# Optimization experiments

Hardware: AMD Instinct MI355X
Metric: run time of the kernel (lower is better)

## Reference

```python
import jax, jax.numpy as jnp
import numpy as np

H = 16
D_MODEL = 1024
D_K = D_MODEL // H


def setup_inputs() -> dict:
    key = jax.random.key(0)
    ks = jax.random.split(key, 8)
    B, S = 4, 2048
    query = jax.random.normal(ks[0], (B, S, D_MODEL), dtype=jnp.float32)
    key_t = jax.random.normal(ks[1], (B, S, D_MODEL), dtype=jnp.float32)
    value = jax.random.normal(ks[2], (B, S, D_MODEL), dtype=jnp.float32)
    mask = jax.random.randint(ks[3], (B, S, S), 0, 2, dtype=jnp.int32)
    sc = 1.0 / np.sqrt(D_MODEL)
    Wq = jax.random.normal(ks[4], (D_MODEL, D_MODEL), dtype=jnp.float32) * sc
    Wk = jax.random.normal(ks[5], (D_MODEL, D_MODEL), dtype=jnp.float32) * sc
    Wv = jax.random.normal(ks[6], (D_MODEL, D_MODEL), dtype=jnp.float32) * sc
    Wo = jax.random.normal(ks[7], (D_MODEL, D_MODEL), dtype=jnp.float32) * sc
    return {"query": query, "key": key_t, "value": value, "mask": mask,
            "Wq": Wq, "Wk": Wk, "Wv": Wv, "Wo": Wo}


def reference(query, key, value, mask, Wq, Wk, Wv, Wo):
    B, S, _ = query.shape
    # nn.Linear(bias=False): y = x @ W^T; then split heads -> [B,H,S,d_k]
    def proj(x, W):
        return (x @ W.T).reshape(B, S, H, D_K).transpose(0, 2, 1, 3)

    q = proj(query, Wq)
    k = proj(key, Wk)
    v = proj(value, Wv)

    m = (mask[:, None, :, :] != 0)  # [B,1,S,S] broadcast over heads
    scores = jnp.einsum('bhqd,bhkd->bhqk', q, k) / jnp.sqrt(jnp.float32(D_K))
    scores = jnp.where(m, scores, jnp.float32(-1e9))
    p_attn = jax.nn.softmax(scores, axis=-1)
    p_attn = jnp.where(m, p_attn, 0.0)
    # dropout is identity in eval mode
    x = jnp.einsum('bhqk,bhkd->bhqd', p_attn, v)
    x = x.transpose(0, 2, 1, 3).reshape(B, S, D_MODEL)
    return x @ Wo.T
```

## Files before the change

### kernel.cpp

```cpp
#include <hip/hip_runtime.h>


typedef __attribute__((ext_vector_type(8))) short frag8;
typedef __attribute__((ext_vector_type(4))) float f32x4;
typedef unsigned long long ull;

#define MFMA16(a,b,c) __builtin_amdgcn_mfma_f32_16x16x32_bf16((a),(b),(c),0,0,0)

__device__ __forceinline__ short f2bf(float f) {
  union { float f; unsigned u; } x; x.f = f;
  unsigned r = (x.u + 0x7fffu + ((x.u >> 16) & 1u)) >> 16;
  return (short)r;
}

__device__ __forceinline__ unsigned pkbf(float lo, float hi) {
  union { float f; unsigned u; } a, b;
  a.f = lo; b.f = hi;
  return __builtin_amdgcn_perm(b.u + 0x8000u, a.u + 0x8000u, 0x07060302u);
}

__device__ __forceinline__ void gl16(const void* g, void* l) {
  __builtin_amdgcn_global_load_lds(
      (const __attribute__((address_space(1))) unsigned*)g,
      (__attribute__((address_space(3))) unsigned*)l, 16, 0, 0);
}

__global__ __launch_bounds__(256) void cast_qkv(
    const float* __restrict__ q, const float* __restrict__ k,
    const float* __restrict__ v, short* __restrict__ qo,
    short* __restrict__ ko, short* __restrict__ vo) {
  int z = blockIdx.x >> 13;
  int i = (blockIdx.x & 8191) * 256 + threadIdx.x;
  const float* s = z == 0 ? q : z == 1 ? k : v;
  short* d = z == 0 ? qo : z == 1 ? ko : vo;
  float4 f = ((const float4*)s)[i];
  short4 o;
  o.x = f2bf(f.x); o.y = f2bf(f.y); o.z = f2bf(f.z); o.w = f2bf(f.w);
  ((short4*)d)[i] = o;
}

__global__ __launch_bounds__(256) void cast_w(
    const float* __restrict__ wq, const float* __restrict__ wk,
    const float* __restrict__ wv, const float* __restrict__ wo,
    short* __restrict__ oq, short* __restrict__ ok,
    short* __restrict__ ov, short* __restrict__ oo) {
  int z = blockIdx.x >> 10;
  int i = (blockIdx.x & 1023) * 256 + threadIdx.x;
  const float* s = z == 0 ? wq : z == 1 ? wk : z == 2 ? wv : wo;
  short* d = z == 0 ? oq : z == 1 ? ok : z == 2 ? ov : oo;
  float sc = (z == 0) ? 0.18033688011f : 1.0f;
  float4 f = ((const float4*)s)[i];
  short4 o;
  o.x = f2bf(f.x * sc); o.y = f2bf(f.y * sc);
  o.z = f2bf(f.z * sc); o.w = f2bf(f.w * sc);
  ((short4*)d)[i] = o;
}

__global__ __launch_bounds__(256) void mask_expand(
    const int* __restrict__ mask, uint2* __restrict__ mexp) {
  int bgrp = blockIdx.x >> 2;
  int kq = blockIdx.x & 3;
  int b = bgrp >> 6, g = bgrp & 63;
  int t = threadIdx.x;
  int l = t & 63, nb = t >> 6;
  int lg = l >> 4, lr = l & 15;
#pragma unroll
  for (int qb = 0; qb < 2; ++qb) {
    const int* row = mask + ((size_t)b * 2048 + g * 32 + qb * 16 + lr) * 2048;
#pragma unroll
    for (int i = 0; i < 8; ++i) {
      int kt = kq * 8 + i;
      int4 m = *(const int4*)(row + kt * 64 + nb * 16 + lg * 4);
      uint2 w;
      w.x = (m.x ? 0xFFFFu : 0u) | (m.y ? 0xFFFF0000u : 0u);
      w.y = (m.z ? 0xFFFFu : 0u) | (m.w ? 0xFFFF0000u : 0u);
      mexp[((size_t)bgrp * 32 + kt) * 512 + (qb * 4 + nb) * 64 + l] = w;
    }
  }
}

template <int MODE>
__device__ __forceinline__ void gemm_body(const short* __restrict__ A,
                                          const short* __restrict__ W,
                                          void* __restrict__ outp, int bid) {
  __shared__ short As[2][128 * 32];
  __shared__ short Bs[2][128 * 32];
  const int t = threadIdx.x;
  const int l = t & 63, wv = t >> 6;
  const int lg = l >> 4, lr = l & 15;
  const int wm = (wv >> 1) * 64, wn = (wv & 1) * 64;
  const int m0 = (bid >> 3) * 128;
  const int n0 = (bid & 7) * 128;

  auto stage = [&](int buf, int kt) {
    const int k0 = kt * 32;
#pragma unroll
    for (int c = 0; c < 2; ++c) {
      int idx = c * 256 + t;
      int row = idx >> 2, ch = (idx & 3) * 8;
      gl16(A + (size_t)(m0 + row) * 1024 + k0 + ch, &As[buf][idx * 8]);
      gl16(W + (size_t)(n0 + row) * 1024 + k0 + ch, &Bs[buf][idx * 8]);
    }
  };

  f32x4 acc[4][4] = {};
  stage(0, 0);
  asm volatile("s_waitcnt vmcnt(0)" ::: "memory");
  __syncthreads();
  int buf = 0;
  for (int kt = 0; kt < 32; ++kt) {
    if (kt + 1 < 32) stage(buf ^ 1, kt + 1);
    frag8 af[4], bf[4];
#pragma unroll
    for (int i = 0; i < 4; ++i) {
      af[i] = *(const frag8*)&As[buf][(wm + i * 16 + lr) * 32 + 8 * lg];
      bf[i] = *(const frag8*)&Bs[buf][(wn + i * 16 + lr) * 32 + 8 * lg];
    }
    __builtin_amdgcn_s_setprio(1);
#pragma unroll
    for (int mi = 0; mi < 4; ++mi)
#pragma unroll
      for (int ni = 0; ni < 4; ++ni)
        acc[mi][ni] = MFMA16(af[mi], bf[ni], acc[mi][ni]);
    __builtin_amdgcn_s_setprio(0);
    asm volatile("s_waitcnt vmcnt(0)" ::: "memory");
    __syncthreads();
    buf ^= 1;
  }

#pragma unroll
  for (int mi = 0; mi < 4; ++mi)
#pragma unroll
    for (int ni = 0; ni < 4; ++ni)
#pragma unroll
      for (int r = 0; r < 4; ++r) {
        int m = m0 + wm + mi * 16 + 4 * lg + r;
        int n = n0 + wn + ni * 16 + lr;
        if (MODE == 0) {
          int b = m >> 11, s = m & 2047, h = n >> 6, dk = n & 63;
          ((short*)outp)[(((size_t)b * 16 + h) * 2048 + s) * 64 + dk] =
              f2bf(acc[mi][ni][r]);
        } else {
          ((float*)outp)[(size_t)m * 1024 + n] = acc[mi][ni][r];
        }
      }
}

__global__ __launch_bounds__(256) void gemm_qkv(
    const short* __restrict__ A0, const short* __restrict__ A1,
    const short* __restrict__ A2, const short* __restrict__ W0,
    const short* __restrict__ W1, const short* __restrict__ W2,
    short* __restrict__ O0, short* __restrict__ O1, short* __restrict__ O2) {
  int wg = (blockIdx.x & 7) * 192 + (blockIdx.x >> 3);
  int z = wg >> 9, bid = wg & 511;
  const short* A = z == 0 ? A0 : z == 1 ? A1 : A2;
  const short* W = z == 0 ? W0 : z == 1 ? W1 : W2;
  short* O = z == 0 ? O0 : z == 1 ? O1 : O2;
  gemm_body<0>(A, W, O, bid);
}

__global__ __launch_bounds__(256) void gemm_o(
    const short* __restrict__ A, const short* __restrict__ W,
    float* __restrict__ O) {
  int bid = (blockIdx.x & 7) * 64 + (blockIdx.x >> 3);
  gemm_body<1>(A, W, O, bid);
}

__global__ __launch_bounds__(256) void transpose_v(
    const short* __restrict__ Vp, short* __restrict__ Vt) {
  __shared__ short lds[64 * 72];
  int bh = blockIdx.y, s0 = blockIdx.x * 64;
  int t = threadIdx.x;
  int rr = t >> 3, c0 = (t & 7) * 8;
#pragma unroll
  for (int half = 0; half < 2; ++half) {
    int r = half * 32 + rr;
    frag8 v = *(const frag8*)(Vp + ((size_t)bh * 2048 + s0 + r) * 64 + c0);
#pragma unroll
    for (int j = 0; j < 8; ++j) lds[r * 72 + c0 + j] = v[j];
  }
  __syncthreads();
#pragma unroll
  for (int half = 0; half < 2; ++half) {
    int d = half * 32 + rr;
    frag8 o;
#pragma unroll
    for (int j = 0; j < 8; ++j) o[j] = lds[(c0 + j) * 72 + d];
    *(frag8*)(Vt + ((size_t)bh * 64 + d) * 2048 + s0 + c0) = o;
  }
}

__global__ __launch_bounds__(256, 4) void attn_fwd(
    const short* __restrict__ Qp, const short* __restrict__ Kp,
    const short* __restrict__ Vt, const uint2* __restrict__ mexp,
    short* __restrict__ X) {
  __shared__ short Ks[2][64 * 64];
  __shared__ short Vs[64 * 64];
  __shared__ short Ps[4][32 * 64];

  const int wg = (blockIdx.x & 7) * 128 + (blockIdx.x >> 3);
  const int qt = wg & 15, bh = wg >> 4;
  const int b = bh >> 4, h = bh & 15;
  const int t = threadIdx.x;
  const int l = t & 63, wv = t >> 6;
  const int lg = l >> 4, lr = l & 15;
  const int q0 = qt * 128 + wv * 32;
  const int qrow_base = b << 11;

  frag8 qf[2][2];
  const short* Qb = Qp + ((size_t)bh * 2048 + q0) * 64;
#pragma unroll
  for (int qb = 0; qb < 2; ++qb)
#pragma unroll
    for (int kc = 0; kc < 2; ++kc)
      qf[qb][kc] = *(const frag8*)(Qb + (qb * 16 + lr) * 64 + kc * 32 + 8 * lg);

  f32x4 acc[4][2] = {};
  float mrun[2] = {0.f, 0.f}, lrun[2] = {0.f, 0.f};

  const size_t kbase = (size_t)bh * 2048 * 64;
  const size_t vbase = (size_t)bh * 64 * 2048;
  short* Pw = &Ps[wv][0];
  const int sx = lr & 7;
  const uint2* mrow = mexp + ((size_t)(b * 64 + qt * 4 + wv) * 32) * 512 + l;

  auto stageK = [&](int buf, int kt) {
#pragma unroll
    for (int p = 0; p < 2; ++p) {
      int idx = p * 256 + t;
      int row = idx >> 3, c = idx & 7;
      int cs = (c ^ (row & 7)) * 8;
      gl16(Kp + kbase + (size_t)(kt * 64 + row) * 64 + cs, &Ks[buf][idx * 8]);
    }
  };
  auto stageV = [&](int kt) {
#pragma unroll
    for (int p = 0; p < 2; ++p) {
      int idx = p * 256 + t;
      int row = idx >> 3, c = idx & 7;
      int cs = (c ^ (row & 7)) * 8;
      gl16(Vt + vbase + (size_t)row * 2048 + kt * 64 + cs, &Vs[idx * 8]);
    }
  };

  stageK(0, 0);
  asm volatile("s_waitcnt vmcnt(0)" ::: "memory");
  __syncthreads();
  int buf = 0;

  for (int kt = 0; kt < 32; ++kt) {
    uint2 mk[2][4];
    const uint2* mt = mrow + kt * 512;
#pragma unroll
    for (int qb = 0; qb < 2; ++qb)
#pragma unroll
      for (int nb = 0; nb < 4; ++nb) mk[qb][nb] = mt[(qb * 4 + nb) * 64];
    asm volatile("" ::: "memory");
    stageV(kt);
    asm volatile("" ::: "memory");
    stageK(buf ^ 1, (kt + 1) & 31);

    f32x4 s[4][2] = {};
    __builtin_amdgcn_s_setprio(1);
#pragma unroll
    for (int nb = 0; nb < 4; ++nb) {
      const int ro = (nb * 16 + lr) * 64;
      frag8 k0 = *(const frag8*)&Ks[buf][ro + ((0 + lg) ^ sx) * 8];
      frag8 k1 = *(const frag8*)&Ks[buf][ro + ((4 + lg) ^ sx) * 8];
#pragma unroll
      for (int qb = 0; qb < 2; ++qb) {
        s[nb][qb] = MFMA16(k0, qf[qb][0], s[nb][qb]);
        s[nb][qb] = MFMA16(k1, qf[qb][1], s[nb][qb]);
      }
    }
    __builtin_amdgcn_s_setprio(0);

#pragma unroll
    for (int qb = 0; qb < 2; ++qb) {
      float tm = -1e30f;
#pragma unroll
      for (int nb = 0; nb < 4; ++nb)
        tm = fmaxf(tm, fmaxf(fmaxf(s[nb][qb][0], s[nb][qb][1]),
                             fmaxf(s[nb][qb][2], s[nb][qb][3])));
      tm = fmaxf(tm, __shfl_xor(tm, 16));
      tm = fmaxf(tm, __shfl_xor(tm, 32));
      float mn = mrun[qb];
      float fac = 1.f;
      bool resc = !__all(tm - mn <= 11.0f);
      if (resc) {
        mn = fmaxf(mn, tm);
        fac = __builtin_amdgcn_exp2f(mrun[qb] - mn);
        mrun[qb] = mn;
      }
      float ts = 0.f;
      const int q64 = (qb * 16 + lr) * 64;
#pragma unroll
      for (int nb = 0; nb < 4; ++nb) {
        float e0 = __builtin_amdgcn_exp2f(s[nb][qb][0] - mn);
        float e1 = __builtin_amdgcn_exp2f(s[nb][qb][1] - mn);
        float e2 = __builtin_amdgcn_exp2f(s[nb][qb][2] - mn);
        float e3 = __builtin_amdgcn_exp2f(s[nb][qb][3] - mn);
        unsigned w0 = pkbf(e0, e1) & mk[qb][nb].x;
        unsigned w1 = pkbf(e2, e3) & mk[qb][nb].y;
        ts += __uint_as_float(w0 << 16) + __uint_as_float(w0 & 0xFFFF0000u) +
              __uint_as_float(w1 << 16) + __uint_as_float(w1 & 0xFFFF0000u);
        uint2 w; w.x = w0; w.y = w1;
        int sw = ((2 * nb + (lg >> 1)) ^ sx) * 8 + 4 * (lg & 1);
        *(uint2*)&Pw[q64 + sw] = w;
      }
      ts += __shfl_xor(ts, 16);
      ts += __shfl_xor(ts, 32);
      if (resc) {
        lrun[qb] = lrun[qb] * fac + ts;
#pragma unroll
        for (int db = 0; db < 4; ++db)
#pragma unroll
          for (int j = 0; j < 4; ++j) acc[db][qb][j] *= fac;
      } else {
        lrun[qb] += ts;
      }
    }

    asm volatile("s_waitcnt vmcnt(2)" ::: "memory");
    __syncthreads();

    frag8 pf[2][2];
#pragma unroll
    for (int qb = 0; qb < 2; ++qb)
#pragma unroll
      for (int kc = 0; kc < 2; ++kc)
        pf[qb][kc] = *(const frag8*)&Pw[(qb * 16 + lr) * 64 +
                                        ((kc * 4 + lg) ^ sx) * 8];
    __builtin_amdgcn_s_setprio(1);
#pragma unroll
    for (int db = 0; db < 4; ++db) {
      const int ro = (db * 16 + lr) * 64;
      frag8 v0 = *(const frag8*)&Vs[ro + ((0 + lg) ^ sx) * 8];
      frag8 v1 = *(const frag8*)&Vs[ro + ((4 + lg) ^ sx) * 8];
#pragma unroll
      for (int qb = 0; qb < 2; ++qb) {
        acc[db][qb] = MFMA16(v0, pf[qb][0], acc[db][qb]);
        acc[db][qb] = MFMA16(v1, pf[qb][1], acc[db][qb]);
      }
    }
    __builtin_amdgcn_s_setprio(0);

    asm volatile("s_waitcnt vmcnt(0)" ::: "memory");
    __syncthreads();
    buf ^= 1;
  }

#pragma unroll
  for (int qb = 0; qb < 2; ++qb) {
    float inv = 1.0f / fmaxf(lrun[qb], 1e-30f);
    int q = q0 + qb * 16 + lr;
    size_t base = (size_t)(qrow_base + q) * 1024 + h * 64 + 4 * lg;
#pragma unroll
    for (int db = 0; db < 4; ++db) {
      uint2 o;
      o.x = pkbf(acc[db][qb][0] * inv, acc[db][qb][1] * inv);
      o.y = pkbf(acc[db][qb][2] * inv, acc[db][qb][3] * inv);
      *(uint2*)&X[base + db * 16] = o;
    }
  }
}

extern "C" void kernel_launch(void* const* d_in, const int* in_sizes, int n_in,
                              void* d_out, int out_size, void* d_ws,
                              size_t ws_size, hipStream_t stream) {
  const float* q  = (const float*)d_in[0];
  const float* k  = (const float*)d_in[1];
  const float* v  = (const float*)d_in[2];
  const int*  msk = (const int*)d_in[3];
  const float* Wq = (const float*)d_in[4];
  const float* Wk = (const float*)d_in[5];
  const float* Wv = (const float*)d_in[6];
  const float* Wo = (const float*)d_in[7];

  const size_t SZ_T = 16777216;
  const size_t SZ_W = 2097152;
  char* ws = (char*)d_ws;
  short* qb  = (short*)(ws + 0 * SZ_T);
  short* kb  = (short*)(ws + 1 * SZ_T);
  short* vb  = (short*)(ws + 2 * SZ_T);
  short* Qp  = (short*)(ws + 3 * SZ_T);
  short* Kp  = (short*)(ws + 4 * SZ_T);
  short* Vp  = (short*)(ws + 5 * SZ_T);
  short* Vt  = (short*)(ws + 6 * SZ_T);
  short* X   = (short*)(ws + 7 * SZ_T);
  short* wqb = (short*)(ws + 8 * SZ_T);
  short* wkb = (short*)(ws + 8 * SZ_T + 1 * SZ_W);
  short* wvb = (short*)(ws + 8 * SZ_T + 2 * SZ_W);
  short* wob = (short*)(ws + 8 * SZ_T + 3 * SZ_W);
  void*  mexp = (void*)(ws + 0 * SZ_T);
  if (ws_size < 8 * SZ_T + 4 * SZ_W) return;

  cast_qkv<<<24576, 256, 0, stream>>>(q, k, v, qb, kb, vb);
  cast_w<<<4096, 256, 0, stream>>>(Wq, Wk, Wv, Wo, wqb, wkb, wvb, wob);
  gemm_qkv<<<1536, 256, 0, stream>>>(qb, kb, vb, wqb, wkb, wvb, Qp, Kp, Vp);
  mask_expand<<<1024, 256, 0, stream>>>(msk, (uint2*)mexp);
  transpose_v<<<dim3(32, 64), 256, 0, stream>>>(Vp, Vt);
  attn_fwd<<<1024, 256, 0, stream>>>(Qp, Kp, Vt, (const uint2*)mexp, X);
  gemm_o<<<512, 256, 0, stream>>>(X, wob, (float*)d_out);
}
```

Before: 289.5 us.

## Register-prefetch K/V tiles and compute softmax row sums with MFMA

Replaces async global->LDS loads and the double-buffered K tile with register-staged prefetch of the next K and V tiles, written to a single LDS buffer between two barriers. The softmax denominator is now accumulated by an extra MFMA of a ones vector against the P fragments, instead of scalar adds and cross-lane shuffles. bf16 packing of P switches to truncation. This frees LDS and removes VALU reduction work, at the cost of more registers, an extra barrier per tile and slightly different rounding.

```diff
diff --git a/kernel.cpp b/kernel.cpp
--- a/kernel.cpp
+++ b/kernel.cpp
@@ -17,6 +17,12 @@
   union { float f; unsigned u; } a, b;
   a.f = lo; b.f = hi;
   return __builtin_amdgcn_perm(b.u + 0x8000u, a.u + 0x8000u, 0x07060302u);
+}
+
+__device__ __forceinline__ unsigned pkbf_t(float lo, float hi) {
+  union { float f; unsigned u; } a, b;
+  a.f = lo; b.f = hi;
+  return __builtin_amdgcn_perm(b.u, a.u, 0x07060302u);
 }
 
 __device__ __forceinline__ void gl16(const void* g, void* l) {
@@ -194,7 +200,7 @@
     const short* __restrict__ Qp, const short* __restrict__ Kp,
     const short* __restrict__ Vt, const uint2* __restrict__ mexp,
     short* __restrict__ X) {
-  __shared__ short Ks[2][64 * 64];
+  __shared__ short Ks[64 * 64];
   __shared__ short Vs[64 * 64];
   __shared__ short Ps[4][32 * 64];
 
@@ -216,57 +222,55 @@
       qf[qb][kc] = *(const frag8*)(Qb + (qb * 16 + lr) * 64 + kc * 32 + 8 * lg);
 
   f32x4 acc[4][2] = {};
-  float mrun[2] = {0.f, 0.f}, lrun[2] = {0.f, 0.f};
-
-  const size_t kbase = (size_t)bh * 2048 * 64;
-  const size_t vbase = (size_t)bh * 64 * 2048;
+  f32x4 accl[2] = {};
+  float mrun[2] = {0.f, 0.f};
+
+  const short* Kg = Kp + (size_t)bh * 2048 * 64;
+  const short* Vg = Vt + (size_t)bh * 64 * 2048;
   short* Pw = &Ps[wv][0];
   const int sx = lr & 7;
   const uint2* mrow = mexp + ((size_t)(b * 64 + qt * 4 + wv) * 32) * 512 + l;
 
-  auto stageK = [&](int buf, int kt) {
-#pragma unroll
-    for (int p = 0; p < 2; ++p) {
-      int idx = p * 256 + t;
-      int row = idx >> 3, c = idx & 7;
-      int cs = (c ^ (row & 7)) * 8;
-      gl16(Kp + kbase + (size_t)(kt * 64 + row) * 64 + cs, &Ks[buf][idx * 8]);
-    }
-  };
-  auto stageV = [&](int kt) {
-#pragma unroll
-    for (int p = 0; p < 2; ++p) {
-      int idx = p * 256 + t;
-      int row = idx >> 3, c = idx & 7;
-      int cs = (c ^ (row & 7)) * 8;
-      gl16(Vt + vbase + (size_t)row * 2048 + kt * 64 + cs, &Vs[idx * 8]);
-    }
-  };
-
-  stageK(0, 0);
-  asm volatile("s_waitcnt vmcnt(0)" ::: "memory");
+  const int r0 = t >> 3, c0 = t & 7;
+  const int r1 = (256 + t) >> 3, c1 = t & 7;
+  const int lk0 = r0 * 64 + ((c0 ^ (r0 & 7)) * 8);
+  const int lk1 = r1 * 64 + ((c1 ^ (r1 & 7)) * 8);
+
+  frag8 ones;
+#pragma unroll
+  for (int j = 0; j < 8; ++j) ones[j] = (short)0x3F80;
+
+  {
+    uint4 ka = *(const uint4*)(Kg + (size_t)r0 * 64 + c0 * 8);
+    uint4 kb_ = *(const uint4*)(Kg + (size_t)r1 * 64 + c1 * 8);
+    uint4 va = *(const uint4*)(Vg + (size_t)r0 * 2048 + c0 * 8);
+    uint4 vb_ = *(const uint4*)(Vg + (size_t)r1 * 2048 + c1 * 8);
+    *(uint4*)&Ks[lk0] = ka; *(uint4*)&Ks[lk1] = kb_;
+    *(uint4*)&Vs[lk0] = va; *(uint4*)&Vs[lk1] = vb_;
+  }
   __syncthreads();
-  int buf = 0;
 
   for (int kt = 0; kt < 32; ++kt) {
+    const int nk = (kt + 1) & 31;
+    uint4 ksa = *(const uint4*)(Kg + (size_t)(nk * 64 + r0) * 64 + c0 * 8);
+    uint4 ksb = *(const uint4*)(Kg + (size_t)(nk * 64 + r1) * 64 + c1 * 8);
+    uint4 vsa = *(const uint4*)(Vg + (size_t)r0 * 2048 + nk * 64 + c0 * 8);
+    uint4 vsb = *(const uint4*)(Vg + (size_t)r1 * 2048 + nk * 64 + c1 * 8);
+
     uint2 mk[2][4];
     const uint2* mt = mrow + kt * 512;
 #pragma unroll
     for (int qb = 0; qb < 2; ++qb)
 #pragma unroll
       for (int nb = 0; nb < 4; ++nb) mk[qb][nb] = mt[(qb * 4 + nb) * 64];
-    asm volatile("" ::: "memory");
-    stageV(kt);
-    asm volatile("" ::: "memory");
-    stageK(buf ^ 1, (kt + 1) & 31);
 
     f32x4 s[4][2] = {};
     __builtin_amdgcn_s_setprio(1);
 #pragma unroll
     for (int nb = 0; nb < 4; ++nb) {
       const int ro = (nb * 16 + lr) * 64;
-      frag8 k0 = *(const frag8*)&Ks[buf][ro + ((0 + lg) ^ sx) * 8];
-      frag8 k1 = *(const frag8*)&Ks[buf][ro + ((4 + lg) ^ sx) * 8];
+      frag8 k0 = *(const frag8*)&Ks[ro + ((0 + lg) ^ sx) * 8];
+      frag8 k1 = *(const frag8*)&Ks[ro + ((4 + lg) ^ sx) * 8];
 #pragma unroll
       for (int qb = 0; qb < 2; ++qb) {
         s[nb][qb] = MFMA16(k0, qf[qb][0], s[nb][qb]);
@@ -285,14 +289,19 @@
       tm = fmaxf(tm, __shfl_xor(tm, 16));
       tm = fmaxf(tm, __shfl_xor(tm, 32));
       float mn = mrun[qb];
-      float fac = 1.f;
       bool resc = !__all(tm - mn <= 11.0f);
       if (resc) {
+        float old = mn;
         mn = fmaxf(mn, tm);
-        fac = __builtin_amdgcn_exp2f(mrun[qb] - mn);
+        float fac = __builtin_amdgcn_exp2f(old - mn);
         mrun[qb] = mn;
+#pragma unroll
+        for (int db = 0; db < 4; ++db)
+#pragma unroll
+          for (int j = 0; j < 4; ++j) acc[db][qb][j] *= fac;
+#pragma unroll
+        for (int j = 0; j < 4; ++j) accl[qb][j] *= fac;
       }
-      float ts = 0.f;
       const int q64 = (qb * 16 + lr) * 64;
 #pragma unroll
       for (int nb = 0; nb < 4; ++nb) {
@@ -300,29 +309,13 @@
         float e1 = __builtin_amdgcn_exp2f(s[nb][qb][1] - mn);
         float e2 = __builtin_amdgcn_exp2f(s[nb][qb][2] - mn);
         float e3 = __builtin_amdgcn_exp2f(s[nb][qb][3] - mn);
-        unsigned w0 = pkbf(e0, e1) & mk[qb][nb].x;
-        unsigned w1 = pkbf(e2, e3) & mk[qb][nb].y;
-        ts += __uint_as_float(w0 << 16) + __uint_as_float(w0 & 0xFFFF0000u) +
-              __uint_as_float(w1 << 16) + __uint_as_float(w1 & 0xFFFF0000u);
-        uint2 w; w.x = w0; w.y = w1;
+        uint2 w;
+        w.x = pkbf_t(e0, e1) & mk[qb][nb].x;
+        w.y = pkbf_t(e2, e3) & mk[qb][nb].y;
         int sw = ((2 * nb + (lg >> 1)) ^ sx) * 8 + 4 * (lg & 1);
         *(uint2*)&Pw[q64 + sw] = w;
       }
-      ts += __shfl_xor(ts, 16);
-      ts += __shfl_xor(ts, 32);
-      if (resc) {
-        lrun[qb] = lrun[qb] * fac + ts;
-#pragma unroll
-        for (int db = 0; db < 4; ++db)
-#pragma unroll
-          for (int j = 0; j < 4; ++j) acc[db][qb][j] *= fac;
-      } else {
-        lrun[qb] += ts;
-      }
-    }
-
-    asm volatile("s_waitcnt vmcnt(2)" ::: "memory");
-    __syncthreads();
+    }
 
     frag8 pf[2][2];
 #pragma unroll
@@ -343,16 +336,22 @@
         acc[db][qb] = MFMA16(v1, pf[qb][1], acc[db][qb]);
       }
     }
+#pragma unroll
+    for (int qb = 0; qb < 2; ++qb) {
+      accl[qb] = MFMA16(ones, pf[qb][0], accl[qb]);
+      accl[qb] = MFMA16(ones, pf[qb][1], accl[qb]);
+    }
     __builtin_amdgcn_s_setprio(0);
 
-    asm volatile("s_waitcnt vmcnt(0)" ::: "memory");
     __syncthreads();
-    buf ^= 1;
+    *(uint4*)&Ks[lk0] = ksa; *(uint4*)&Ks[lk1] = ksb;
+    *(uint4*)&Vs[lk0] = vsa; *(uint4*)&Vs[lk1] = vsb;
+    __syncthreads();
   }
 
 #pragma unroll
   for (int qb = 0; qb < 2; ++qb) {
-    float inv = 1.0f / fmaxf(lrun[qb], 1e-30f);
+    float inv = 1.0f / fmaxf(accl[qb][0], 1e-30f);
     int q = q0 + qb * 16 + lr;
     size_t base = (size_t)(qrow_base + q) * 1024 + h * 64 + 4 * lg;
 #pragma unroll
```

New measurement: 366.0 us. 26.4% more time.

## Compute softmax row sums with MFMA against ones and halve P scratch

Applied to the files above, without the earlier changes.

The per-iteration softmax denominator, previously built with VALU adds and cross-lane shuffles, is now accumulated by extra MFMAs that multiply the masked bf16 P tile by a vector of ones. The P scratch buffer in LDS is halved so the two 16-row query blocks reuse one slice: block 0's fragments are read back before block 1 is written. The bf16 packing for P switches from rounding to truncation. Together these cut VALU and shuffle work and LDS footprint, at the cost of four extra MFMAs per tile, a more serial softmax-then-read sequence, and slightly different numerics from truncation.

```diff
diff --git a/kernel.cpp b/kernel.cpp
--- a/kernel.cpp
+++ b/kernel.cpp
@@ -17,6 +17,12 @@
   union { float f; unsigned u; } a, b;
   a.f = lo; b.f = hi;
   return __builtin_amdgcn_perm(b.u + 0x8000u, a.u + 0x8000u, 0x07060302u);
+}
+
+__device__ __forceinline__ unsigned pkbf_t(float lo, float hi) {
+  union { float f; unsigned u; } a, b;
+  a.f = lo; b.f = hi;
+  return __builtin_amdgcn_perm(b.u, a.u, 0x07060302u);
 }
 
 __device__ __forceinline__ void gl16(const void* g, void* l) {
@@ -196,7 +202,7 @@
     short* __restrict__ X) {
   __shared__ short Ks[2][64 * 64];
   __shared__ short Vs[64 * 64];
-  __shared__ short Ps[4][32 * 64];
+  __shared__ short Ps[4][16 * 64];
 
   const int wg = (blockIdx.x & 7) * 128 + (blockIdx.x >> 3);
   const int qt = wg & 15, bh = wg >> 4;
@@ -216,7 +222,8 @@
       qf[qb][kc] = *(const frag8*)(Qb + (qb * 16 + lr) * 64 + kc * 32 + 8 * lg);
 
   f32x4 acc[4][2] = {};
-  float mrun[2] = {0.f, 0.f}, lrun[2] = {0.f, 0.f};
+  f32x4 accl[2] = {};
+  float mrun[2] = {0.f, 0.f};
 
   const size_t kbase = (size_t)bh * 2048 * 64;
   const size_t vbase = (size_t)bh * 64 * 2048;
@@ -224,6 +231,10 @@
   const int sx = lr & 7;
   const uint2* mrow = mexp + ((size_t)(b * 64 + qt * 4 + wv) * 32) * 512 + l;
 
+  frag8 ones;
+#pragma unroll
+  for (int j = 0; j < 8; ++j) ones[j] = (short)0x3F80;
+
   auto stageK = [&](int buf, int kt) {
 #pragma unroll
     for (int p = 0; p < 2; ++p) {
@@ -275,8 +286,7 @@
     }
     __builtin_amdgcn_s_setprio(0);
 
-#pragma unroll
-    for (int qb = 0; qb < 2; ++qb) {
+    auto softmax_store = [&](int qb) {
       float tm = -1e30f;
 #pragma unroll
       for (int nb = 0; nb < 4; ++nb)
@@ -285,64 +295,63 @@
       tm = fmaxf(tm, __shfl_xor(tm, 16));
       tm = fmaxf(tm, __shfl_xor(tm, 32));
       float mn = mrun[qb];
-      float fac = 1.f;
       bool resc = !__all(tm - mn <= 11.0f);
       if (resc) {
+        float old = mn;
         mn = fmaxf(mn, tm);
-        fac = __builtin_amdgcn_exp2f(mrun[qb] - mn);
+        float fac = __builtin_amdgcn_exp2f(old - mn);
         mrun[qb] = mn;
+#pragma unroll
+        for (int db = 0; db < 4; ++db)
+#pragma unroll
+          for (int j = 0; j < 4; ++j) acc[db][qb][j] *= fac;
+#pragma unroll
+        for (int j = 0; j < 4; ++j) accl[qb][j] *= fac;
       }
-      float ts = 0.f;
-      const int q64 = (qb * 16 + lr) * 64;
+      const int q64 = lr * 64;
 #pragma unroll
       for (int nb = 0; nb < 4; ++nb) {
         float e0 = __builtin_amdgcn_exp2f(s[nb][qb][0] - mn);
         float e1 = __builtin_amdgcn_exp2f(s[nb][qb][1] - mn);
         float e2 = __builtin_amdgcn_exp2f(s[nb][qb][2] - mn);
         float e3 = __builtin_amdgcn_exp2f(s[nb][qb][3] - mn);
-        unsigned w0 = pkbf(e0, e1) & mk[qb][nb].x;
-        unsigned w1 = pkbf(e2, e3) & mk[qb][nb].y;
-        ts += __uint_as_float(w0 << 16) + __uint_as_float(w0 & 0xFFFF0000u) +
-              __uint_as_float(w1 << 16) + __uint_as_float(w1 & 0xFFFF0000u);
-        uint2 w; w.x = w0; w.y = w1;
+        uint2 w;
+        w.x = pkbf_t(e0, e1) & mk[qb][nb].x;
+        w.y = pkbf_t(e2, e3) & mk[qb][nb].y;
         int sw = ((2 * nb + (lg >> 1)) ^ sx) * 8 + 4 * (lg & 1);
         *(uint2*)&Pw[q64 + sw] = w;
       }
-      ts += __shfl_xor(ts, 16);
-      ts += __shfl_xor(ts, 32);
-      if (resc) {
-        lrun[qb] = lrun[qb] * fac + ts;
-#pragma unroll
-        for (int db = 0; db < 4; ++db)
-#pragma unroll
-          for (int j = 0; j < 4; ++j) acc[db][qb][j] *= fac;
-      } else {
-        lrun[qb] += ts;
-      }
-    }
+    };
+
+    softmax_store(0);
 
     asm volatile("s_waitcnt vmcnt(2)" ::: "memory");
     __syncthreads();
 
-    frag8 pf[2][2];
-#pragma unroll
-    for (int qb = 0; qb < 2; ++qb)
-#pragma unroll
-      for (int kc = 0; kc < 2; ++kc)
-        pf[qb][kc] = *(const frag8*)&Pw[(qb * 16 + lr) * 64 +
-                                        ((kc * 4 + lg) ^ sx) * 8];
+    frag8 pf0[2], pf1[2];
+#pragma unroll
+    for (int kc = 0; kc < 2; ++kc)
+      pf0[kc] = *(const frag8*)&Pw[lr * 64 + ((kc * 4 + lg) ^ sx) * 8];
+    softmax_store(1);
+#pragma unroll
+    for (int kc = 0; kc < 2; ++kc)
+      pf1[kc] = *(const frag8*)&Pw[lr * 64 + ((kc * 4 + lg) ^ sx) * 8];
+
     __builtin_amdgcn_s_setprio(1);
 #pragma unroll
     for (int db = 0; db < 4; ++db) {
       const int ro = (db * 16 + lr) * 64;
       frag8 v0 = *(const frag8*)&Vs[ro + ((0 + lg) ^ sx) * 8];
       frag8 v1 = *(const frag8*)&Vs[ro + ((4 + lg) ^ sx) * 8];
-#pragma unroll
-      for (int qb = 0; qb < 2; ++qb) {
-        acc[db][qb] = MFMA16(v0, pf[qb][0], acc[db][qb]);
-        acc[db][qb] = MFMA16(v1, pf[qb][1], acc[db][qb]);
-      }
-    }
+      acc[db][0] = MFMA16(v0, pf0[0], acc[db][0]);
+      acc[db][0] = MFMA16(v1, pf0[1], acc[db][0]);
+      acc[db][1] = MFMA16(v0, pf1[0], acc[db][1]);
+      acc[db][1] = MFMA16(v1, pf1[1], acc[db][1]);
+    }
+    accl[0] = MFMA16(ones, pf0[0], accl[0]);
+    accl[0] = MFMA16(ones, pf0[1], accl[0]);
+    accl[1] = MFMA16(ones, pf1[0], accl[1]);
+    accl[1] = MFMA16(ones, pf1[1], accl[1]);
     __builtin_amdgcn_s_setprio(0);
 
     asm volatile("s_waitcnt vmcnt(0)" ::: "memory");
@@ -352,7 +361,7 @@
 
 #pragma unroll
   for (int qb = 0; qb < 2; ++qb) {
-    float inv = 1.0f / fmaxf(lrun[qb], 1e-30f);
+    float inv = 1.0f / fmaxf(accl[qb][0], 1e-30f);
     int q = q0 + qb * 16 + lr;
     size_t base = (size_t)(qrow_base + q) * 1024 + h * 64 + 4 * lg;
 #pragma unroll
```

Measured after the change: 293.4 us. Within noise of the previous version (+1.3%).
